# Performance work log

Hardware: AMD Instinct MI355X
Metric: run time of the kernel (lower is better)

## Reference

```python
import jax, jax.numpy as jnp
import numpy as np


def _diff_x(x, r):
    # x: [..., Hp, W]; sliding-window difference of column-cumsum along axis -2
    left = x[..., r:2 * r + 1, :]
    middle = x[..., 2 * r + 1:, :] - x[..., :-2 * r - 1, :]
    right = x[..., -1:, :] - x[..., -2 * r - 1:-r - 1, :]
    return jnp.concatenate([left, middle, right], axis=-2)


def _diff_y(x, r):
    # x: [..., H, Wp]; sliding-window difference along axis -1
    left = x[..., r:2 * r + 1]
    middle = x[..., 2 * r + 1:] - x[..., :-2 * r - 1]
    right = x[..., -1:] - x[..., -2 * r - 1:-r - 1]
    return jnp.concatenate([left, middle, right], axis=-1)


def setup_inputs() -> dict:
    key = jax.random.key(0)
    B, C, H, W = 8, 3, 2048, 2048
    x = jax.random.normal(key, (B, C, H, W), dtype=jnp.float32)
    return {"x": x, "r": 4}


def reference(x, r):
    # reflect pad r on both spatial dims (PyTorch 'reflect' == numpy 'reflect')
    xp = jnp.pad(x, ((0, 0), (0, 0), (r, r), (r, r)), mode="reflect")
    xp = jnp.cumsum(xp, axis=-2)
    xp = _diff_x(xp, r)
    xp = jnp.cumsum(xp, axis=-1)
    xp = _diff_y(xp, r)
    norm = jnp.asarray((2 * r + 1) ** 2, dtype=x.dtype)
    return xp[..., r:-r, r:-r] / norm
```

## Files before the change

kernel.cpp:

```cpp
#include <hip/hip_runtime.h>


constexpr int H   = 2048;
constexpr int W   = 2048;
constexpr int R   = 4;
constexpr int RH  = 32;
constexpr int TPB = 256;
constexpr int CPT = 4;
constexpr int BCOLS = TPB * CPT;

typedef float f32x4 __attribute__((ext_vector_type(4)));

__device__ __forceinline__ int reflect_row(int r) {
  r = (r < 0) ? -r : r;
  return (r >= H) ? (2 * H - 2 - r) : r;
}

template <int P, bool STORE>
__device__ __forceinline__ void bf_step(
    int s, int r0, int off, int c0,
    const float* __restrict__ px, float* __restrict__ po,
    float (&hbuf)[9][CPT], float (&vsum)[CPT]) {
  const int lr = reflect_row(r0 - R + s);
  const float* __restrict__ rowp = px + (size_t)lr * W;

  const float4 A = *(const float4*)(rowp + off);
  const float4 B = *(const float4*)(rowp + off + 4);
  const float4 C = *(const float4*)(rowp + off + 8);

  float h0 = ((A.x + A.y) + (A.z + A.w)) +
             ((B.x + B.y) + (B.z + B.w)) + C.x;
  float h1 = h0 + C.y - A.x;
  float h2 = h1 + C.z - A.y;
  float h3 = h2 + C.w - A.z;

  vsum[0] += h0 - hbuf[P][0]; hbuf[P][0] = h0;
  vsum[1] += h1 - hbuf[P][1]; hbuf[P][1] = h1;
  vsum[2] += h2 - hbuf[P][2]; hbuf[P][2] = h2;
  vsum[3] += h3 - hbuf[P][3]; hbuf[P][3] = h3;

  if (STORE) {
    const float inv81 = 1.0f / 81.0f;
    float* o = po + (size_t)(r0 + s - 2 * R) * W + c0;
    f32x4 ov = {vsum[0] * inv81, vsum[1] * inv81,
                vsum[2] * inv81, vsum[3] * inv81};
    __builtin_nontemporal_store(ov, (f32x4*)o);
  }
}

__global__ __launch_bounds__(TPB, 5) void BoxFilter_kernel(
    const float* __restrict__ x, float* __restrict__ out) {
  const int t    = threadIdx.x;
  const int bid  = blockIdx.x;
  const int plane = bid >> 7;
  const int rem   = bid & 127;
  const int chunk = rem >> 1;
  const int half  = rem & 1;
  const int r0    = chunk * RH;
  const int cb    = half * BCOLS;
  const float* __restrict__ px = x   + (size_t)plane * H * W;
  float*       __restrict__ po = out + (size_t)plane * H * W;

  const int c0 = cb + t * CPT;
  int off = c0 - R;
  off = off < 0 ? 0 : off;
  off = off > W - 12 ? W - 12 : off;

  float hbuf[9][CPT];
  float vsum[CPT];
#pragma unroll
  for (int j = 0; j < CPT; ++j) vsum[j] = 0.0f;
#pragma unroll
  for (int p = 0; p < 9; ++p)
#pragma unroll
    for (int j = 0; j < CPT; ++j) hbuf[p][j] = 0.0f;

  bf_step<0, false>(0, r0, off, c0, px, po, hbuf, vsum);
  bf_step<1, false>(1, r0, off, c0, px, po, hbuf, vsum);
  bf_step<2, false>(2, r0, off, c0, px, po, hbuf, vsum);
  bf_step<3, false>(3, r0, off, c0, px, po, hbuf, vsum);
  bf_step<4, false>(4, r0, off, c0, px, po, hbuf, vsum);
  bf_step<5, false>(5, r0, off, c0, px, po, hbuf, vsum);
  bf_step<6, false>(6, r0, off, c0, px, po, hbuf, vsum);
  bf_step<7, false>(7, r0, off, c0, px, po, hbuf, vsum);
  bf_step<8, true>(8, r0, off, c0, px, po, hbuf, vsum);

#pragma unroll 1
  for (int s0 = 9; s0 <= 27; s0 += 9) {
    bf_step<0, true>(s0 + 0, r0, off, c0, px, po, hbuf, vsum);
    bf_step<1, true>(s0 + 1, r0, off, c0, px, po, hbuf, vsum);
    bf_step<2, true>(s0 + 2, r0, off, c0, px, po, hbuf, vsum);
    bf_step<3, true>(s0 + 3, r0, off, c0, px, po, hbuf, vsum);
    bf_step<4, true>(s0 + 4, r0, off, c0, px, po, hbuf, vsum);
    bf_step<5, true>(s0 + 5, r0, off, c0, px, po, hbuf, vsum);
    bf_step<6, true>(s0 + 6, r0, off, c0, px, po, hbuf, vsum);
    bf_step<7, true>(s0 + 7, r0, off, c0, px, po, hbuf, vsum);
    bf_step<8, true>(s0 + 8, r0, off, c0, px, po, hbuf, vsum);
  }
  bf_step<0, true>(36, r0, off, c0, px, po, hbuf, vsum);
  bf_step<1, true>(37, r0, off, c0, px, po, hbuf, vsum);
  bf_step<2, true>(38, r0, off, c0, px, po, hbuf, vsum);
  bf_step<3, true>(39, r0, off, c0, px, po, hbuf, vsum);
}

__global__ __launch_bounds__(TPB) void edge_fix(
    const float* __restrict__ x, float* __restrict__ out) {
  const int idx = blockIdx.x * blockDim.x + threadIdx.x;
  const int plane = idx >> 11;
  const int r     = idx & (H - 1);
  const float* __restrict__ px = x   + (size_t)plane * H * W;
  float*       __restrict__ po = out + (size_t)plane * H * W;

  float accL[4] = {0.f, 0.f, 0.f, 0.f};
  float accR[4] = {0.f, 0.f, 0.f, 0.f};

#pragma unroll
  for (int dr = -R; dr <= R; ++dr) {
    const int rr = reflect_row(r + dr);
    const float* __restrict__ rowp = px + (size_t)rr * W;
    float l[9], m[9];
#pragma unroll
    for (int i = 0; i < 9; ++i) l[i] = rowp[i];
#pragma unroll
    for (int i = 0; i < 9; ++i) m[i] = rowp[W - 9 + i];
#pragma unroll
    for (int c = 0; c < 4; ++c) {
#pragma unroll
      for (int k = -R; k <= R; ++k) {
        int j = c + k; j = (j < 0) ? -j : j;
        accL[c] += l[j];
        int rc = (W - 4 + c) + k;
        rc = (rc >= W) ? (2 * W - 2 - rc) : rc;
        accR[c] += m[rc - (W - 9)];
      }
    }
  }

  const float inv81 = 1.0f / 81.0f;
  float* oL = po + (size_t)r * W;
  float* oR = po + (size_t)r * W + (W - 4);
  f32x4 vL = {accL[0] * inv81, accL[1] * inv81, accL[2] * inv81, accL[3] * inv81};
  f32x4 vR = {accR[0] * inv81, accR[1] * inv81, accR[2] * inv81, accR[3] * inv81};
  *(f32x4*)oL = vL;
  *(f32x4*)oR = vR;
}

extern "C" void kernel_launch(void* const* d_in, const int* in_sizes, int n_in,
                              void* d_out, int out_size, void* d_ws, size_t ws_size,
                              hipStream_t stream) {
  const float* x   = (const float*)d_in[0];
  float*       out = (float*)d_out;
  const int planes = out_size / (H * W);
  dim3 grid(planes * (H / RH) * 2);
  dim3 block(TPB);
  hipLaunchKernelGGL(BoxFilter_kernel, grid, block, 0, stream, x, out);
  dim3 fgrid(planes * H / TPB);
  hipLaunchKernelGGL(edge_fix, fgrid, block, 0, stream, x, out);
}
```

Measured before the change: 173.4 us.

## Fuse edge-fix into main box filter launch, double row chunk, remap blocks

```diff
diff --git a/kernel.cpp b/kernel.cpp
--- a/kernel.cpp
+++ b/kernel.cpp
@@ -4,7 +4,7 @@
 constexpr int H   = 2048;
 constexpr int W   = 2048;
 constexpr int R   = 4;
-constexpr int RH  = 32;
+constexpr int RH  = 64;
 constexpr int TPB = 256;
 constexpr int CPT = 4;
 constexpr int BCOLS = TPB * CPT;
@@ -18,7 +18,7 @@
 
 template <int P, bool STORE>
 __device__ __forceinline__ void bf_step(
-    int s, int r0, int off, int c0,
+    int s, int r0, int off, int c0, bool doStore,
     const float* __restrict__ px, float* __restrict__ po,
     float (&hbuf)[9][CPT], float (&vsum)[CPT]) {
   const int lr = reflect_row(r0 - R + s);
@@ -40,22 +40,68 @@
   vsum[3] += h3 - hbuf[P][3]; hbuf[P][3] = h3;
 
   if (STORE) {
-    const float inv81 = 1.0f / 81.0f;
-    float* o = po + (size_t)(r0 + s - 2 * R) * W + c0;
-    f32x4 ov = {vsum[0] * inv81, vsum[1] * inv81,
-                vsum[2] * inv81, vsum[3] * inv81};
-    __builtin_nontemporal_store(ov, (f32x4*)o);
+    if (doStore) {
+      const float inv81 = 1.0f / 81.0f;
+      float* o = po + (size_t)(r0 + s - 2 * R) * W + c0;
+      f32x4 ov = {vsum[0] * inv81, vsum[1] * inv81,
+                  vsum[2] * inv81, vsum[3] * inv81};
+      __builtin_nontemporal_store(ov, (f32x4*)o);
+    }
   }
 }
 
 __global__ __launch_bounds__(TPB, 5) void BoxFilter_kernel(
-    const float* __restrict__ x, float* __restrict__ out) {
-  const int t    = threadIdx.x;
-  const int bid  = blockIdx.x;
-  const int plane = bid >> 7;
-  const int rem   = bid & 127;
-  const int chunk = rem >> 1;
-  const int half  = rem & 1;
+    const float* __restrict__ x, float* __restrict__ out, int nMain) {
+  const int t   = threadIdx.x;
+  const int bid = blockIdx.x;
+
+  if (bid >= nMain) {
+    const int idx   = (bid - nMain) * TPB + t;
+    const int plane = idx >> 11;
+    const int r     = idx & (H - 1);
+    const float* __restrict__ px = x   + (size_t)plane * H * W;
+    float*       __restrict__ po = out + (size_t)plane * H * W;
+
+    float accL[4] = {0.f, 0.f, 0.f, 0.f};
+    float accR[4] = {0.f, 0.f, 0.f, 0.f};
+#pragma unroll
+    for (int dr = -R; dr <= R; ++dr) {
+      const int rr = reflect_row(r + dr);
+      const float* __restrict__ rowp = px + (size_t)rr * W;
+      float l[9], m[9];
+#pragma unroll
+      for (int i = 0; i < 9; ++i) l[i] = rowp[i];
+#pragma unroll
+      for (int i = 0; i < 9; ++i) m[i] = rowp[W - 9 + i];
+#pragma unroll
+      for (int c = 0; c < 4; ++c) {
+#pragma unroll
+        for (int k = -R; k <= R; ++k) {
+          int j = c + k; j = (j < 0) ? -j : j;
+          accL[c] += l[j];
+          int rc = (W - 4 + c) + k;
+          rc = (rc >= W) ? (2 * W - 2 - rc) : rc;
+          accR[c] += m[rc - (W - 9)];
+        }
+      }
+    }
+    const float inv81 = 1.0f / 81.0f;
+    float* oL = po + (size_t)r * W;
+    float* oR = po + (size_t)r * W + (W - 4);
+    f32x4 vL = {accL[0] * inv81, accL[1] * inv81,
+                accL[2] * inv81, accL[3] * inv81};
+    f32x4 vR = {accR[0] * inv81, accR[1] * inv81,
+                accR[2] * inv81, accR[3] * inv81};
+    *(f32x4*)oL = vL;
+    *(f32x4*)oR = vR;
+    return;
+  }
+
+  const int lid   = (bid & 7) * (nMain >> 3) + (bid >> 3);
+  const int plane = lid >> 6;
+  const int rem   = lid & 63;
+  const int half  = rem >> 5;
+  const int chunk = rem & 31;
   const int r0    = chunk * RH;
   const int cb    = half * BCOLS;
   const float* __restrict__ px = x   + (size_t)plane * H * W;
@@ -65,6 +111,7 @@
   int off = c0 - R;
   off = off < 0 ? 0 : off;
   off = off > W - 12 ? W - 12 : off;
+  const bool doStore = (c0 != 0) && (c0 != W - CPT);
 
   float hbuf[9][CPT];
   float vsum[CPT];
@@ -75,74 +122,28 @@
 #pragma unroll
     for (int j = 0; j < CPT; ++j) hbuf[p][j] = 0.0f;
 
-  bf_step<0, false>(0, r0, off, c0, px, po, hbuf, vsum);
-  bf_step<1, false>(1, r0, off, c0, px, po, hbuf, vsum);
-  bf_step<2, false>(2, r0, off, c0, px, po, hbuf, vsum);
-  bf_step<3, false>(3, r0, off, c0, px, po, hbuf, vsum);
-  bf_step<4, false>(4, r0, off, c0, px, po, hbuf, vsum);
-  bf_step<5, false>(5, r0, off, c0, px, po, hbuf, vsum);
-  bf_step<6, false>(6, r0, off, c0, px, po, hbuf, vsum);
-  bf_step<7, false>(7, r0, off, c0, px, po, hbuf, vsum);
-  bf_step<8, true>(8, r0, off, c0, px, po, hbuf, vsum);
+  bf_step<0, false>(0, r0, off, c0, doStore, px, po, hbuf, vsum);
+  bf_step<1, false>(1, r0, off, c0, doStore, px, po, hbuf, vsum);
+  bf_step<2, false>(2, r0, off, c0, doStore, px, po, hbuf, vsum);
+  bf_step<3, false>(3, r0, off, c0, doStore, px, po, hbuf, vsum);
+  bf_step<4, false>(4, r0, off, c0, doStore, px, po, hbuf, vsum);
+  bf_step<5, false>(5, r0, off, c0, doStore, px, po, hbuf, vsum);
+  bf_step<6, false>(6, r0, off, c0, doStore, px, po, hbuf, vsum);
+  bf_step<7, false>(7, r0, off, c0, doStore, px, po, hbuf, vsum);
+  bf_step<8, true>(8, r0, off, c0, doStore, px, po, hbuf, vsum);
 
 #pragma unroll 1
-  for (int s0 = 9; s0 <= 27; s0 += 9) {
-    bf_step<0, true>(s0 + 0, r0, off, c0, px, po, hbuf, vsum);
-    bf_step<1, true>(s0 + 1, r0, off, c0, px, po, hbuf, vsum);
-    bf_step<2, true>(s0 + 2, r0, off, c0, px, po, hbuf, vsum);
-    bf_step<3, true>(s0 + 3, r0, off, c0, px, po, hbuf, vsum);
-    bf_step<4, true>(s0 + 4, r0, off, c0, px, po, hbuf, vsum);
-    bf_step<5, true>(s0 + 5, r0, off, c0, px, po, hbuf, vsum);
-    bf_step<6, true>(s0 + 6, r0, off, c0, px, po, hbuf, vsum);
-    bf_step<7, true>(s0 + 7, r0, off, c0, px, po, hbuf, vsum);
-    bf_step<8, true>(s0 + 8, r0, off, c0, px, po, hbuf, vsum);
+  for (int s0 = 9; s0 <= 63; s0 += 9) {
+    bf_step<0, true>(s0 + 0, r0, off, c0, doStore, px, po, hbuf, vsum);
+    bf_step<1, true>(s0 + 1, r0, off, c0, doStore, px, po, hbuf, vsum);
+    bf_step<2, true>(s0 + 2, r0, off, c0, doStore, px, po, hbuf, vsum);
+    bf_step<3, true>(s0 + 3, r0, off, c0, doStore, px, po, hbuf, vsum);
+    bf_step<4, true>(s0 + 4, r0, off, c0, doStore, px, po, hbuf, vsum);
+    bf_step<5, true>(s0 + 5, r0, off, c0, doStore, px, po, hbuf, vsum);
+    bf_step<6, true>(s0 + 6, r0, off, c0, doStore, px, po, hbuf, vsum);
+    bf_step<7, true>(s0 + 7, r0, off, c0, doStore, px, po, hbuf, vsum);
+    bf_step<8, true>(s0 + 8, r0, off, c0, doStore, px, po, hbuf, vsum);
   }
-  bf_step<0, true>(36, r0, off, c0, px, po, hbuf, vsum);
-  bf_step<1, true>(37, r0, off, c0, px, po, hbuf, vsum);
-  bf_step<2, true>(38, r0, off, c0, px, po, hbuf, vsum);
-  bf_step<3, true>(39, r0, off, c0, px, po, hbuf, vsum);
-}
-
-__global__ __launch_bounds__(TPB) void edge_fix(
-    const float* __restrict__ x, float* __restrict__ out) {
-  const int idx = blockIdx.x * blockDim.x + threadIdx.x;
-  const int plane = idx >> 11;
-  const int r     = idx & (H - 1);
-  const float* __restrict__ px = x   + (size_t)plane * H * W;
-  float*       __restrict__ po = out + (size_t)plane * H * W;
-
-  float accL[4] = {0.f, 0.f, 0.f, 0.f};
-  float accR[4] = {0.f, 0.f, 0.f, 0.f};
-
-#pragma unroll
-  for (int dr = -R; dr <= R; ++dr) {
-    const int rr = reflect_row(r + dr);
-    const float* __restrict__ rowp = px + (size_t)rr * W;
-    float l[9], m[9];
-#pragma unroll
-    for (int i = 0; i < 9; ++i) l[i] = rowp[i];
-#pragma unroll
-    for (int i = 0; i < 9; ++i) m[i] = rowp[W - 9 + i];
-#pragma unroll
-    for (int c = 0; c < 4; ++c) {
-#pragma unroll
-      for (int k = -R; k <= R; ++k) {
-        int j = c + k; j = (j < 0) ? -j : j;
-        accL[c] += l[j];
-        int rc = (W - 4 + c) + k;
-        rc = (rc >= W) ? (2 * W - 2 - rc) : rc;
-        accR[c] += m[rc - (W - 9)];
-      }
-    }
-  }
-
-  const float inv81 = 1.0f / 81.0f;
-  float* oL = po + (size_t)r * W;
-  float* oR = po + (size_t)r * W + (W - 4);
-  f32x4 vL = {accL[0] * inv81, accL[1] * inv81, accL[2] * inv81, accL[3] * inv81};
-  f32x4 vR = {accR[0] * inv81, accR[1] * inv81, accR[2] * inv81, accR[3] * inv81};
-  *(f32x4*)oL = vL;
-  *(f32x4*)oR = vR;
 }
 
 extern "C" void kernel_launch(void* const* d_in, const int* in_sizes, int n_in,
@@ -151,9 +152,9 @@
   const float* x   = (const float*)d_in[0];
   float*       out = (float*)d_out;
   const int planes = out_size / (H * W);
-  dim3 grid(planes * (H / RH) * 2);
+  const int nMain  = planes * (H / RH) * 2;
+  const int nEdge  = planes * H / TPB;
+  dim3 grid(nMain + nEdge);
   dim3 block(TPB);
-  hipLaunchKernelGGL(BoxFilter_kernel, grid, block, 0, stream, x, out);
-  dim3 fgrid(planes * H / TPB);
-  hipLaunchKernelGGL(edge_fix, fgrid, block, 0, stream, x, out);
+  hipLaunchKernelGGL(BoxFilter_kernel, grid, block, 0, stream, x, out, nMain);
 }
```

New measurement: 179.4 us. +3.5%, slower.
